# Performance work log

Hardware: AMD Instinct MI355X
Metric: run time of the kernel (lower is better)

Reference implementation:

```python
import jax, jax.numpy as jnp
import numpy as np

NC = 10          # num_clusters
D_MODEL = 512
H = 8
DK = 64          # d_model = H*DK
B = 8
L = 2048


def _mlp2(x, W1, b1, W2, b2):
    h = jax.nn.gelu(x @ W1 + b1, approximate=False)
    return h @ W2 + b2


def setup_inputs() -> dict:
    key = jax.random.key(0)
    ks = jax.random.split(key, 12)
    s_in = 1.0 / np.sqrt(D_MODEL)
    s_h = 1.0 / np.sqrt(4 * NC)
    s_nc = 1.0 / np.sqrt(NC)
    return {
        "Q": jax.random.normal(ks[0], (B, H, L, DK), jnp.float32),
        "K": jax.random.normal(ks[1], (B, H, L, DK), jnp.float32),
        "V": jax.random.normal(ks[2], (B, H, L, DK), jnp.float32),
        # cluster_k_proj: Linear(d_model,4*nc) GELU Linear(4*nc,nc); stored as [in,out]
        "Wk1": jax.random.normal(ks[3], (D_MODEL, 4 * NC), jnp.float32) * s_in,
        "bk1": jnp.zeros((4 * NC,), jnp.float32),
        "Wk2": jax.random.normal(ks[4], (4 * NC, NC), jnp.float32) * s_h,
        "bk2": jnp.zeros((NC,), jnp.float32),
        # cluster_q_proj
        "Wq1": jax.random.normal(ks[5], (D_MODEL, 4 * NC), jnp.float32) * s_in,
        "bq1": jnp.zeros((4 * NC,), jnp.float32),
        "Wq2": jax.random.normal(ks[6], (4 * NC, NC), jnp.float32) * s_h,
        "bq2": jnp.zeros((NC,), jnp.float32),
        # proj_back_to_cluster_k: Linear(nc, d_model) + GELU
        "Wp": jax.random.normal(ks[7], (NC, D_MODEL), jnp.float32) * s_nc,
        "bp": jnp.zeros((D_MODEL,), jnp.float32),
    }


def _forward(Q, K, V, Wk1, bk1, Wk2, bk2, Wq1, bq1, Wq2, bq2, Wp, bp):
    b, h, l, d_k = Q.shape
    nc = Wk2.shape[1]
    unfolding = 10 * nc

    def pool(x):
        # torch: MaxPool1d(kernel=9, stride=9(default), padding=4) on reshape(b, d_k*h, -1)
        x3 = x.reshape(b, d_k * h, -1)
        y = jax.lax.reduce_window(x3, -jnp.inf, jax.lax.max,
                                  (1, 1, 9), (1, 1, 9),
                                  ((0, 0), (0, 0), (4, 4)))
        return y.reshape(b, h, -1, d_k)

    Kp = pool(K)
    Vp = pool(V)
    l_k = Kp.shape[2]

    # pad along batch dim and take sliding windows of size `unfolding` (stride 1)
    pad = jnp.zeros((unfolding, h, l_k, d_k), Kp.dtype)
    K_padded = jnp.concatenate([pad, Kp[1:]], axis=0)      # [unfolding+b-1, h, l_k, d_k]
    idx = jnp.arange(b)[:, None] + jnp.arange(unfolding)[None, :]
    K_unf = K_padded[idx]                                  # [b, unfolding, h, l_k, d_k]
    K_unf = jnp.transpose(K_unf, (0, 2, 3, 4, 1))          # torch unfold puts window last
    K_unf = K_unf.reshape(b, l_k, unfolding, d_k * h)      # row-major reshape, as torch

    ck = jax.nn.softmax(_mlp2(K_unf, Wk1, bk1, Wk2, bk2), axis=-1)  # [b,l_k,u,nc]
    cq = jax.nn.softmax(_mlp2(K_unf, Wq1, bq1, Wq2, bq2), axis=-1)

    mu = jnp.mean(cq, axis=-1)                             # [b, l_k, unfolding]
    sigma = jax.nn.softplus(jnp.std(cq, axis=-1, ddof=1))  # torch std is unbiased
    x = jnp.mean(ck, axis=-1)
    log_prob = -0.5 * jnp.square((x - mu) / sigma) - jnp.log(sigma) - 0.5 * jnp.log(2.0 * jnp.pi)
    # torch CrossEntropyLoss(mu, mu): classes are dim 1 (l_k), soft prob targets
    logp = jax.nn.log_softmax(mu, axis=1)
    ce = jnp.mean(-jnp.sum(mu * logp, axis=1))
    loss = -jnp.mean(log_prob) + ce

    # fused scatter-style cluster centers: mean over window of cq with assigned cluster zeroed
    assign = jnp.argmax(cq, axis=-1)                       # [b, l_k, unfolding]
    onehot = jax.nn.one_hot(assign, nc, dtype=cq.dtype)    # [b, l_k, u, i] (constant wrt grad)
    total = jnp.sum(cq, axis=2)                            # [b, l_k, nc]
    S = jnp.einsum('blui,bluc->blic', onehot, cq)          # sum of cq at masked positions
    centers = (total[:, :, None, :] - S) / unfolding       # [b, l_k, nc_i, nc_c]
    centers = jnp.transpose(centers, (2, 0, 1, 3))         # [nc, b, l_k, nc]

    cc = jax.nn.gelu(centers @ Wp + bp, approximate=False) # [nc, b, l_k, d_model]
    cc = cc.reshape(b, h, nc, l_k, d_k)                    # faithful torch reshape

    scores = jnp.einsum('bhqd,bhckd->bhqk', Q, cc) / np.sqrt(d_k).astype(Q.dtype)
    attn = jax.nn.softmax(scores, axis=-1)
    context = jnp.einsum('bhqk,bhkd->bhqd', attn, Vp)
    return context, loss


def reference(Q, K, V, Wk1, bk1, Wk2, bk2, Wq1, bq1, Wq2, bq2, Wp, bp):
    return _forward(Q, K, V, Wk1, bk1, Wk2, bk2, Wq1, bq1, Wq2, bq2, Wp, bp)
```

## Files before the change

### kernel.cpp

```cpp
#include <hip/hip_runtime.h>
#include <math.h>

#define NCL 10
#define DM 512
#define NH 8
#define DK 64
#define NB 8
#define SL 2048
#define LK 228
#define UF 100
#define KP_PER_B (NH*LK*DK)
#define KP_TOT (NB*KP_PER_B)
#define NROWS (NB*LK*UF)
#define POOL2_BLOCKS 8192

typedef __bf16 bf16_t;
typedef __attribute__((ext_vector_type(2))) __bf16 bf16x2;
typedef __attribute__((ext_vector_type(8))) __bf16 bf16x8;
typedef __attribute__((ext_vector_type(4))) float f32x4;

__device__ __forceinline__ float gelu_f(float x) {
    return 0.5f * x * (1.f + erff(x * 0.70710678118654752f));
}

__global__ void k_pool(const float* __restrict__ K, const float* __restrict__ V,
                       float* __restrict__ Kp, float* __restrict__ Vp,
                       const float* __restrict__ Wq1, bf16_t* __restrict__ W1b,
                       float* __restrict__ acc) {
    int bid = blockIdx.x;
    int tid = threadIdx.x;
    if (bid >= POOL2_BLOCKS) {
        int i = (bid - POOL2_BLOCKS) * 256 + tid;
        if (i < 512 * 40) W1b[i] = (bf16_t)Wq1[i];
        if (bid == POOL2_BLOCKS && tid < 4) acc[tid] = 0.f;
        return;
    }
    int kv = bid >> 12;
    int e0 = bid & 4095;
    int b = e0 >> 9;
    int c = e0 & 511;
    const float* src = kv ? V : K;
    float* dst = kv ? Vp : Kp;
    __shared__ float buf[2048];
    const float* base = src + (size_t)e0 * 2048;
    #pragma unroll
    for (int i = 0; i < 2; ++i) {
        int i4 = (tid + i * 256) << 2;
        *(float4*)&buf[i4] = *(const float4*)&base[i4];
    }
    __syncthreads();
    if (tid < LK) {
        int p0 = tid * 9 - 4;
        float mx = -3.4e38f;
        #pragma unroll
        for (int j = 0; j < 9; ++j) {
            int p = p0 + j;
            if (p >= 0 && p < 2048) mx = fmaxf(mx, buf[p]);
        }
        dst[b * KP_PER_B + c * LK + tid] = mx;
    }
}

template<int B>
__device__ __forceinline__ void layer1(int tid, const bf16_t* __restrict__ W1b,
                                       const float* __restrict__ Sstf,
                                       float* __restrict__ hT) {
    #pragma unroll 1
    for (int k = 0; k < 2; ++k) {
        int vt = tid + (k << 8);
        if (vt < 500) {
            int m = vt / 5;
            int h8 = vt - m * 5;
            int bm = (12 * m) % 100;
            float h[8];
            #pragma unroll
            for (int i = 0; i < 8; ++i) h[i] = 0.f;
            #pragma unroll
            for (int s = 1; s <= B; ++s) {
                const int t = 99 - B + s;
                int d0 = t - bm; if (d0 < 0) d0 += 100;
                int r0 = ((m << 9) + d0 - t) / 100;
                const float* srow = &Sstf[s << 9];
                #pragma unroll
                for (int j = 0; j < 6; ++j) {
                    int c = d0 + j * 100;
                    if (j < 5 || c < 512) {
                        float v = srow[r0 + j];
                        bf16x8 w = *(const bf16x8*)&W1b[c * 40 + h8 * 8];
                        #pragma unroll
                        for (int i = 0; i < 8; ++i)
                            h[i] = fmaf(v, (float)w[i], h[i]);
                    }
                }
            }
            #pragma unroll
            for (int i = 0; i < 8; ++i) hT[m * 44 + h8 * 8 + i] = h[i];
        }
    }
}

__global__ __launch_bounds__(256, 4) void k_mlp(
        const float* __restrict__ Kp, const bf16_t* __restrict__ W1b,
        const float* __restrict__ bq1,
        const float* __restrict__ Wq2, const float* __restrict__ bq2,
        float* __restrict__ mu_g, float* __restrict__ centers_g,
        float* __restrict__ acc_g) {
    __shared__ __align__(16) char smem[34432];
    float* Sstf  = (float*)smem;
    float* hT    = (float*)(smem + 16384);
    float* stats = (float*)(smem + 33984);

    int tid = threadIdx.x;
    int bl = blockIdx.x;
    int b = bl / LK;
    int l = bl % LK;

    for (int s4 = tid; s4 < 128 * b; s4 += 256) {
        int bk = (s4 >> 7) + 1;
        int r4 = (s4 & 127) << 2;
        *(float4*)&Sstf[(bk << 9) + r4] =
            *(const float4*)&Kp[bk * KP_PER_B + l * 512 + r4];
    }
    if (tid < 111) stats[tid] = 0.f;
    if (b == 0) {
        for (int i = tid; i < 4400; i += 256) hT[i] = 0.f;
    }
    __syncthreads();

    switch (b) {
        case 1: layer1<1>(tid, W1b, Sstf, hT); break;
        case 2: layer1<2>(tid, W1b, Sstf, hT); break;
        case 3: layer1<3>(tid, W1b, Sstf, hT); break;
        case 4: layer1<4>(tid, W1b, Sstf, hT); break;
        case 5: layer1<5>(tid, W1b, Sstf, hT); break;
        case 6: layer1<6>(tid, W1b, Sstf, hT); break;
        case 7: layer1<7>(tid, W1b, Sstf, hT); break;
        default: break;
    }
    __syncthreads();

    for (int i = tid; i < 4000; i += 256) {
        int row = i / 40;
        int j = i - row * 40;
        hT[row * 44 + j] = gelu_f(hT[row * 44 + j] + bq1[j]);
    }
    __syncthreads();

    float* total_l = stats;
    float* S_l = stats + 10;
    float* lp_acc = stats + 110;

    if (tid < 100) {
        int row = tid;
        float g[40];
        #pragma unroll
        for (int j4 = 0; j4 < 10; ++j4) {
            float4 gv = *(const float4*)&hT[row * 44 + j4 * 4];
            g[j4 * 4 + 0] = gv.x; g[j4 * 4 + 1] = gv.y;
            g[j4 * 4 + 2] = gv.z; g[j4 * 4 + 3] = gv.w;
        }
        float out[10];
        #pragma unroll
        for (int c = 0; c < 10; ++c) out[c] = bq2[c];
        #pragma unroll
        for (int j = 0; j < 40; ++j) {
            float gj = g[j];
            #pragma unroll
            for (int c = 0; c < 10; ++c)
                out[c] = fmaf(gj, Wq2[j * 10 + c], out[c]);
        }
        float m = out[0]; int am = 0;
        #pragma unroll
        for (int c = 1; c < 10; ++c)
            if (out[c] > m) { m = out[c]; am = c; }
        float e[10], s = 0.f;
        #pragma unroll
        for (int c = 0; c < 10; ++c) { e[c] = expf(out[c] - m); s += e[c]; }
        float inv = 1.f / s;
        float cq[10], s1 = 0.f;
        #pragma unroll
        for (int c = 0; c < 10; ++c) { cq[c] = e[c] * inv; s1 += cq[c]; }
        float mean = s1 * 0.1f;
        float var = 0.f;
        #pragma unroll
        for (int c = 0; c < 10; ++c) { float d = cq[c] - mean; var += d * d; }
        float sd = sqrtf(var / 9.f);
        float sp = log1pf(expf(sd));
        float lp = -logf(sp) - 0.91893853320467274f;
        mu_g[bl * 100 + row] = mean;
        atomicAdd(lp_acc, lp);
        #pragma unroll
        for (int c = 0; c < 10; ++c) {
            atomicAdd(&total_l[c], cq[c]);
            atomicAdd(&S_l[am * 10 + c], cq[c]);
        }
    }
    __syncthreads();
    if (tid == 0) atomicAdd(&acc_g[0], lp_acc[0]);
    if (tid < 100) {
        centers_g[bl * 100 + tid] = (total_l[tid % 10] - S_l[tid]) * 0.01f;
    }
}

__global__ void k_ce(const float* __restrict__ mu_g, float* __restrict__ acc_g,
                     float* __restrict__ outp) {
    int bid = blockIdx.x;
    int b = bid / 100;
    int u = bid % 100;
    int lane = threadIdx.x;
    float v[4];
    #pragma unroll
    for (int t = 0; t < 4; ++t) {
        int l = lane + t * 64;
        v[t] = (l < LK) ? mu_g[(b * LK + l) * 100 + u] : -3.4e38f;
    }
    float m = fmaxf(fmaxf(v[0], v[1]), fmaxf(v[2], v[3]));
    for (int o = 32; o > 0; o >>= 1) m = fmaxf(m, __shfl_xor(m, o, 64));
    float se = 0.f;
    #pragma unroll
    for (int t = 0; t < 4; ++t) {
        int l = lane + t * 64;
        if (l < LK) se += expf(v[t] - m);
    }
    for (int o = 32; o > 0; o >>= 1) se += __shfl_xor(se, o, 64);
    float lse = m + logf(se);
    float dot = 0.f;
    #pragma unroll
    for (int t = 0; t < 4; ++t) {
        int l = lane + t * 64;
        if (l < LK) dot += v[t] * (v[t] - lse);
    }
    for (int o = 32; o > 0; o >>= 1) dot += __shfl_xor(dot, o, 64);
    if (lane == 0) {
        atomicAdd(&acc_g[1], -dot * (1.f / 800.f));
        __threadfence();
        unsigned int old = atomicAdd((unsigned int*)&acc_g[2], 1u);
        if (old == 799u) {
            __threadfence();
            outp[8388608] = -(acc_g[0] * (1.f / (float)NROWS)) + acc_g[1];
        }
    }
}

__global__ void k_ccs(const float* __restrict__ centers_g,
                      const float* __restrict__ Wp, const float* __restrict__ bp,
                      float* __restrict__ ccs) {
    int tid = blockIdx.x * 256 + threadIdx.x;
    if (tid >= KP_TOT) return;
    int k2d2 = tid % (LK * DK);
    int bh = tid / (LK * DK);
    float s = 0.f;
    #pragma unroll
    for (int i2 = 0; i2 < 10; ++i2) {
        int t2 = bh * 145920 + i2 * 14592 + k2d2;
        int i = t2 / 933888;
        int r1 = t2 % 933888;
        int bs = r1 / 116736;
        int r2 = r1 % 116736;
        int ls = r2 / 512;
        int mm = r2 % 512;
        const float* cen = centers_g + (bs * LK + ls) * 100 + i * 10;
        float val = bp[mm];
        #pragma unroll
        for (int c = 0; c < 10; ++c)
            val = fmaf(cen[c], Wp[c * 512 + mm], val);
        s += gelu_f(val);
    }
    ccs[tid] = s;
}

#define QT 128
__global__ __launch_bounds__(256, 3) void k_attn(
        const float* __restrict__ Q, const float* __restrict__ ccs,
        const float* __restrict__ Vp, float* __restrict__ outp) {
    __shared__ __align__(16) char smem[36864];
    bf16_t* Kl = (bf16_t*)(smem);
    bf16_t* Vt = (bf16_t*)(smem + 9216);
    bf16_t* Pl = (bf16_t*)(smem + 18432);

    int tid = threadIdx.x;
    int wid = tid >> 6;
    int lane = tid & 63;
    int ln = lane & 15;
    int qd = lane >> 4;
    int bid = blockIdx.x;
    int bh = bid >> 4;
    int qt = bid & 15;
    int qbase = qt * QT;

    const float* Qbh = Q + (size_t)bh * SL * DK;
    const float* Kbh = ccs + (size_t)bh * LK * DK;
    const float* Vbh = Vp + (size_t)bh * LK * DK;

    for (int s = tid; s < QT * 32; s += 256) {
        int r = s >> 5;
        int c2 = s & 31;
        float2 v = *(const float2*)&Qbh[(size_t)(qbase + r) * DK + c2 * 2];
        *(bf16x2*)&Pl[r * 72 + c2 * 2] = (bf16x2){(bf16_t)v.x, (bf16_t)v.y};
    }
    __syncthreads();
    bf16x8 qf[2][2];
    #pragma unroll
    for (int mt = 0; mt < 2; ++mt)
        #pragma unroll
        for (int ks = 0; ks < 2; ++ks)
            qf[mt][ks] = *(const bf16x8*)&Pl[(wid * 32 + mt * 16 + ln) * 72 + ks * 32 + qd * 8];

    f32x4 acc_o[2][4];
    float mrow[2][4], lrow[2][4];
    #pragma unroll
    for (int mt = 0; mt < 2; ++mt)
        #pragma unroll
        for (int t = 0; t < 4; ++t) {
            acc_o[mt][t] = (f32x4)(0.f);
            mrow[mt][t] = -3.0e38f;
            lrow[mt][t] = 0.f;
        }

    for (int ch = 0; ch < 4; ++ch) {
        int k0 = ch * 64;
        __syncthreads();
        for (int s = tid; s < 64 * 32; s += 256) {
            int kk = s >> 5;
            int c2 = s & 31;
            int key = k0 + kk;
            float2 v = (key < LK) ? *(const float2*)&Kbh[(size_t)key * DK + c2 * 2]
                                  : make_float2(0.f, 0.f);
            *(bf16x2*)&Kl[kk * 72 + c2 * 2] = (bf16x2){(bf16_t)v.x, (bf16_t)v.y};
        }
        for (int s = tid; s < 64 * 16; s += 256) {
            int kk = s >> 4;
            int c4 = s & 15;
            int key = k0 + kk;
            float4 v = (key < LK) ? *(const float4*)&Vbh[(size_t)key * DK + c4 * 4]
                                  : make_float4(0.f, 0.f, 0.f, 0.f);
            Vt[(c4 * 4 + 0) * 72 + kk] = (bf16_t)v.x;
            Vt[(c4 * 4 + 1) * 72 + kk] = (bf16_t)v.y;
            Vt[(c4 * 4 + 2) * 72 + kk] = (bf16_t)v.z;
            Vt[(c4 * 4 + 3) * 72 + kk] = (bf16_t)v.w;
        }
        __syncthreads();

        f32x4 accs[2][4];
        #pragma unroll
        for (int mt = 0; mt < 2; ++mt)
            #pragma unroll
            for (int nt = 0; nt < 4; ++nt) accs[mt][nt] = (f32x4)(0.f);
        #pragma unroll
        for (int ks = 0; ks < 2; ++ks) {
            #pragma unroll
            for (int nt = 0; nt < 4; ++nt) {
                bf16x8 bf = *(const bf16x8*)&Kl[(nt * 16 + ln) * 72 + ks * 32 + qd * 8];
                #pragma unroll
                for (int mt = 0; mt < 2; ++mt)
                    accs[mt][nt] = __builtin_amdgcn_mfma_f32_16x16x32_bf16(qf[mt][ks], bf, accs[mt][nt], 0, 0, 0);
            }
        }

        #pragma unroll
        for (int mt = 0; mt < 2; ++mt) {
            #pragma unroll
            for (int r = 0; r < 4; ++r) {
                float sv[4];
                #pragma unroll
                for (int nt = 0; nt < 4; ++nt) {
                    float s = accs[mt][nt][r] * 0.125f;
                    int key = k0 + nt * 16 + ln;
                    sv[nt] = (key < LK) ? s : -3.0e38f;
                }
                float rmax = fmaxf(fmaxf(sv[0], sv[1]), fmaxf(sv[2], sv[3]));
                #pragma unroll
                for (int o = 1; o < 16; o <<= 1)
                    rmax = fmaxf(rmax, __shfl_xor(rmax, o, 64));
                float mold = mrow[mt][r];
                float mnew = fmaxf(mold, rmax);
                float alpha = __expf(mold - mnew);
                float p[4], psum = 0.f;
                #pragma unroll
                for (int nt = 0; nt < 4; ++nt) {
                    p[nt] = __expf(sv[nt] - mnew);
                    psum += p[nt];
                }
                #pragma unroll
                for (int o = 1; o < 16; o <<= 1)
                    psum += __shfl_xor(psum, o, 64);
                lrow[mt][r] = lrow[mt][r] * alpha + psum;
                mrow[mt][r] = mnew;
                #pragma unroll
                for (int ntv = 0; ntv < 4; ++ntv)
                    acc_o[mt][ntv][r] *= alpha;
                int prow = (wid * 32 + mt * 16 + qd * 4 + r) * 72;
                #pragma unroll
                for (int nt = 0; nt < 4; ++nt)
                    Pl[prow + nt * 16 + ln] = (bf16_t)p[nt];
            }
        }

        #pragma unroll
        for (int ks = 0; ks < 2; ++ks) {
            bf16x8 pa[2];
            #pragma unroll
            for (int mt = 0; mt < 2; ++mt)
                pa[mt] = *(const bf16x8*)&Pl[(wid * 32 + mt * 16 + ln) * 72 + ks * 32 + qd * 8];
            #pragma unroll
            for (int ntv = 0; ntv < 4; ++ntv) {
                bf16x8 vb = *(const bf16x8*)&Vt[(ntv * 16 + ln) * 72 + ks * 32 + qd * 8];
                #pragma unroll
                for (int mt = 0; mt < 2; ++mt)
                    acc_o[mt][ntv] = __builtin_amdgcn_mfma_f32_16x16x32_bf16(pa[mt], vb, acc_o[mt][ntv], 0, 0, 0);
            }
        }
    }

    #pragma unroll
    for (int mt = 0; mt < 2; ++mt) {
        #pragma unroll
        for (int r = 0; r < 4; ++r) {
            float inv = 1.f / lrow[mt][r];
            int q_idx = qbase + wid * 32 + mt * 16 + qd * 4 + r;
            float* orow = outp + ((size_t)bh * SL + q_idx) * DK;
            #pragma unroll
            for (int ntv = 0; ntv < 4; ++ntv)
                orow[ntv * 16 + ln] = acc_o[mt][ntv][r] * inv;
        }
    }
}

extern "C" void kernel_launch(void* const* d_in, const int* in_sizes, int n_in,
                              void* d_out, int out_size, void* d_ws, size_t ws_size,
                              hipStream_t stream) {
    const float* Q   = (const float*)d_in[0];
    const float* K   = (const float*)d_in[1];
    const float* V   = (const float*)d_in[2];
    const float* Wq1 = (const float*)d_in[7];
    const float* bq1 = (const float*)d_in[8];
    const float* Wq2 = (const float*)d_in[9];
    const float* bq2 = (const float*)d_in[10];
    const float* Wp  = (const float*)d_in[11];
    const float* bp  = (const float*)d_in[12];
    float* out = (float*)d_out;

    float* ws      = (float*)d_ws;
    float* Kp      = ws;
    float* Vp      = ws + 933888;
    float* mu      = ws + 1867776;
    float* centers = ws + 2050176;
    float* ccs     = ws + 2232576;
    float* acc     = ws + 3166464;
    bf16_t* W1b    = (bf16_t*)(ws + 3166468);

    k_pool<<<POOL2_BLOCKS + 80, 256, 0, stream>>>(K, V, Kp, Vp, Wq1, W1b, acc);
    k_mlp<<<NB * LK, 256, 0, stream>>>(Kp, W1b, bq1, Wq2, bq2, mu, centers, acc);
    k_ccs<<<(KP_TOT + 255) / 256, 256, 0, stream>>>(centers, Wp, bp, ccs);
    k_ce<<<NB * 100, 64, 0, stream>>>(mu, acc, out);
    k_attn<<<NB * NH * (SL / QT), 256, 0, stream>>>(Q, ccs, Vp, out);
}
```

Before: 331.0 us.

## Compute cluster-q MLP first layer with bf16 MFMA tiles instead of scalar FMAs

Replaces the scalar per-thread layer-1 dot products, which exploited the sparse window structure, with a dense 100x512 by 512x40 bf16 MFMA GEMM per block. W1 is stored transposed in global memory and staged in LDS with padding, and A tiles are gathered from Kp per K-chunk with zeros for padded positions. Bias and GELU are fused into the accumulator writeback. The cost is more LDS (lower occupancy, launch bounds drop to 2), 32 barriers per block, and dense compute even when most inputs are zero (small b).

```diff
diff --git a/kernel.cpp b/kernel.cpp
--- a/kernel.cpp
+++ b/kernel.cpp
@@ -31,7 +31,11 @@
     int tid = threadIdx.x;
     if (bid >= POOL2_BLOCKS) {
         int i = (bid - POOL2_BLOCKS) * 256 + tid;
-        if (i < 512 * 40) W1b[i] = (bf16_t)Wq1[i];
+        if (i < 512 * 40) {
+            int c = i / 40;
+            int n = i - c * 40;
+            W1b[n * 512 + c] = (bf16_t)Wq1[i];
+        }
         if (bid == POOL2_BLOCKS && tid < 4) acc[tid] = 0.f;
         return;
     }
@@ -61,88 +65,102 @@
     }
 }
 
-template<int B>
-__device__ __forceinline__ void layer1(int tid, const bf16_t* __restrict__ W1b,
-                                       const float* __restrict__ Sstf,
-                                       float* __restrict__ hT) {
-    #pragma unroll 1
-    for (int k = 0; k < 2; ++k) {
-        int vt = tid + (k << 8);
-        if (vt < 500) {
-            int m = vt / 5;
-            int h8 = vt - m * 5;
-            int bm = (12 * m) % 100;
-            float h[8];
-            #pragma unroll
-            for (int i = 0; i < 8; ++i) h[i] = 0.f;
-            #pragma unroll
-            for (int s = 1; s <= B; ++s) {
-                const int t = 99 - B + s;
-                int d0 = t - bm; if (d0 < 0) d0 += 100;
-                int r0 = ((m << 9) + d0 - t) / 100;
-                const float* srow = &Sstf[s << 9];
-                #pragma unroll
-                for (int j = 0; j < 6; ++j) {
-                    int c = d0 + j * 100;
-                    if (j < 5 || c < 512) {
-                        float v = srow[r0 + j];
-                        bf16x8 w = *(const bf16x8*)&W1b[c * 40 + h8 * 8];
-                        #pragma unroll
-                        for (int i = 0; i < 8; ++i)
-                            h[i] = fmaf(v, (float)w[i], h[i]);
-                    }
-                }
-            }
-            #pragma unroll
-            for (int i = 0; i < 8; ++i) hT[m * 44 + h8 * 8 + i] = h[i];
-        }
-    }
-}
-
-__global__ __launch_bounds__(256, 4) void k_mlp(
+__global__ __launch_bounds__(256, 2) void k_mlp(
         const float* __restrict__ Kp, const bf16_t* __restrict__ W1b,
         const float* __restrict__ bq1,
         const float* __restrict__ Wq2, const float* __restrict__ bq2,
         float* __restrict__ mu_g, float* __restrict__ centers_g,
         float* __restrict__ acc_g) {
-    __shared__ __align__(16) char smem[34432];
-    float* Sstf  = (float*)smem;
-    float* hT    = (float*)(smem + 16384);
-    float* stats = (float*)(smem + 33984);
+    __shared__ __align__(16) char smem[75968];
+    bf16_t* W1T  = (bf16_t*)smem;
+    bf16_t* A    = (bf16_t*)(smem + 49920);
+    float*  hT   = (float*)(smem + 57920);
+    float*  stats= (float*)(smem + 75520);
 
     int tid = threadIdx.x;
     int bl = blockIdx.x;
     int b = bl / LK;
     int l = bl % LK;
 
-    for (int s4 = tid; s4 < 128 * b; s4 += 256) {
-        int bk = (s4 >> 7) + 1;
-        int r4 = (s4 & 127) << 2;
-        *(float4*)&Sstf[(bk << 9) + r4] =
-            *(const float4*)&Kp[bk * KP_PER_B + l * 512 + r4];
+    int lane = tid & 63;
+    int wid = tid >> 6;
+    int ln = lane & 15;
+    int qd = lane >> 4;
+
+    for (int idx = tid; idx < 48 * 64; idx += 256) {
+        int n = idx >> 6;
+        int c16 = idx & 63;
+        float4 v;
+        if (n < 40)
+            v = *(const float4*)((const char*)W1b + n * 1024 + c16 * 16);
+        else
+            v = make_float4(0.f, 0.f, 0.f, 0.f);
+        *(float4*)((char*)W1T + n * 1040 + c16 * 16) = v;
     }
     if (tid < 111) stats[tid] = 0.f;
-    if (b == 0) {
-        for (int i = tid; i < 4400; i += 256) hT[i] = 0.f;
-    }
+
+    f32x4 acc0[3], acc1[3];
+    #pragma unroll
+    for (int nt = 0; nt < 3; ++nt) { acc0[nt] = (f32x4)(0.f); acc1[nt] = (f32x4)(0.f); }
+    const int mt0 = wid;
+    const int mt1 = wid + 4;
+    const bool has1 = (wid < 3);
+    const int tmin = 100 - b;
+    const float* Kpl = Kp + l * 512;
+
     __syncthreads();
 
-    switch (b) {
-        case 1: layer1<1>(tid, W1b, Sstf, hT); break;
-        case 2: layer1<2>(tid, W1b, Sstf, hT); break;
-        case 3: layer1<3>(tid, W1b, Sstf, hT); break;
-        case 4: layer1<4>(tid, W1b, Sstf, hT); break;
-        case 5: layer1<5>(tid, W1b, Sstf, hT); break;
-        case 6: layer1<6>(tid, W1b, Sstf, hT); break;
-        case 7: layer1<7>(tid, W1b, Sstf, hT); break;
-        default: break;
-    }
-    __syncthreads();
-
-    for (int i = tid; i < 4000; i += 256) {
-        int row = i / 40;
-        int j = i - row * 40;
-        hT[row * 44 + j] = gelu_f(hT[row * 44 + j] + bq1[j]);
+    for (int kc = 0; kc < 16; ++kc) {
+        int c0 = kc * 32;
+        for (int idx = tid; idx < 3200; idx += 256) {
+            int m = idx >> 5;
+            int cc = idx & 31;
+            int g = (m << 9) + c0 + cc;
+            int q = g / 100;
+            int t = g - q * 100;
+            float val = 0.f;
+            if (t >= tmin) {
+                int s = t - 99 + b;
+                val = Kpl[s * KP_PER_B + q];
+            }
+            A[m * 40 + cc] = (bf16_t)val;
+        }
+        __syncthreads();
+        bf16x8 bfr[3];
+        #pragma unroll
+        for (int nt = 0; nt < 3; ++nt)
+            bfr[nt] = *(const bf16x8*)&W1T[(nt * 16 + ln) * 520 + c0 + qd * 8];
+        bf16x8 a0 = *(const bf16x8*)&A[(mt0 * 16 + ln) * 40 + qd * 8];
+        #pragma unroll
+        for (int nt = 0; nt < 3; ++nt)
+            acc0[nt] = __builtin_amdgcn_mfma_f32_16x16x32_bf16(a0, bfr[nt], acc0[nt], 0, 0, 0);
+        if (has1) {
+            bf16x8 a1 = *(const bf16x8*)&A[(mt1 * 16 + ln) * 40 + qd * 8];
+            #pragma unroll
+            for (int nt = 0; nt < 3; ++nt)
+                acc1[nt] = __builtin_amdgcn_mfma_f32_16x16x32_bf16(a1, bfr[nt], acc1[nt], 0, 0, 0);
+        }
+        __syncthreads();
+    }
+
+    #pragma unroll
+    for (int nt = 0; nt < 3; ++nt) {
+        int n = nt * 16 + ln;
+        if (n < 40) {
+            float bn = bq1[n];
+            #pragma unroll
+            for (int r = 0; r < 4; ++r) {
+                int m = mt0 * 16 + qd * 4 + r;
+                if (m < 100) hT[m * 44 + n] = gelu_f(acc0[nt][r] + bn);
+            }
+            if (has1) {
+                #pragma unroll
+                for (int r = 0; r < 4; ++r) {
+                    int m = mt1 * 16 + qd * 4 + r;
+                    if (m < 100) hT[m * 44 + n] = gelu_f(acc1[nt][r] + bn);
+                }
+            }
+        }
     }
     __syncthreads();
 
```

After: 482.7 us. 1.46x slower.
